# Kernel tuning notes

Measured on AMD Instinct MI355X. Metric: run time of the kernel, lower is better.

Reference implementation:

```python
import jax, jax.numpy as jnp
import numpy as np
from jax.scipy.special import gammaln

T, G, M = 730, 2000, 4
NEARZERO = 1e-5
UH_LEN = 15

PHY_NAMES = ['inf_pc','inf_hbv_beta','inf_vic_bexp','inf_hmets_alpha','sr_soil_depth_1',
 'bf1_gr4j_x3','bf1_pl_bfc','bf1_pl_bfn','bf1_vic_bfmax','bf1_vic_bfn','bf1_top_bfmax',
 'bf1_top_bfn','bf1_top_lam','bf1_thresh_bfmax','bf1_thresh_bfn','bf1_thresh_bfthresh',
 'perc_gawser_maxperc','crise_hbv_crise','bf2_con_bfmax','bf2_gr4j_x3','bf2_lin_bfc',
 'bf2_pl_bfc','bf2_pl_bfn','bf2_vic_bfmax','bf2_vic_bfn',
 'ddf','Tbm','Tbf','cfr','swi','vadose_max_level']
PHY_BOUNDS = np.array([[0.,1.],[0.5,3.],[0.001,3.],[0.3,1.],[0.05,0.5],
 [20.,300.],[0.001,0.5],[1.,5.],[0.1,50.],[1.,5.],[0.1,50.],
 [1.,5.],[5.,10.],[0.1,50.],[1.,5.],[0.,1.],
 [1.,50.],[0.1,50.],[0.1,50.],[20.,300.],[0.0001,0.1],
 [0.0001,0.1],[1.,5.],[0.1,50.],[1.,5.],
 [0.,20.],[-2.,3.],[-5.,2.],[0.,1.],[0.05,0.4],[10.,500.]], dtype=np.float32)
ROUT_BOUNDS = np.array([[0.3,20.],[0.01,5.],[0.5,13.],[0.15,1.5]], dtype=np.float32)


def uh_gamma(a, theta, L):
    # gamma-distribution unit hydrograph, a/theta: [G] -> [G, L]
    aa = jax.nn.relu(a) + 0.1
    th = jax.nn.relu(theta) + 0.5
    t = jnp.arange(0.5, float(L))  # [L]
    logw = (aa[:, None] - 1.0) * jnp.log(t)[None, :] - t[None, :] / th[:, None] \
           - gammaln(aa)[:, None] - aa[:, None] * jnp.log(th[:, None])
    w = jnp.exp(logw)
    return w / jnp.sum(w, axis=1, keepdims=True)


def route(q, uh):
    # causal per-basin convolution: q [T,G], uh [G,L] -> [T,G]
    L = uh.shape[1]
    x = q.T[None]                 # [1, G, T]
    k = uh[:, None, ::-1]         # [G, 1, L]  (reversed -> true convolution)
    out = jax.lax.conv_general_dilated(x, k, window_strides=(1,),
                                       padding=[(L - 1, 0)],
                                       feature_group_count=G,
                                       dimension_numbers=('NCW', 'OIW', 'NCW'))
    return out[0].T


def _model(x_phy, weights_params, hybrid_params):
    P = len(PHY_NAMES)
    lb = jnp.asarray(PHY_BOUNDS[:, 0]); ub = jnp.asarray(PHY_BOUNDS[:, 1])
    phy = jax.nn.sigmoid(hybrid_params[:, :P * M].reshape(G, P, M))
    phy = lb[None, :, None] + phy * (ub - lb)[None, :, None]       # [G,P,M]
    pd = {n: phy[:, i, :] for i, n in enumerate(PHY_NAMES)}
    rb = jnp.asarray(ROUT_BOUNDS)
    rout = jax.nn.sigmoid(hybrid_params[:, P * M:P * M + 4])
    rout = rb[:, 0][None] + rout * (rb[:, 1] - rb[:, 0])[None]      # [G,4]
    a1, b1, a2, b2 = rout[:, 0], rout[:, 1], rout[:, 2], rout[:, 3]
    # 9 blend weights, softmax within the 3 groups of 3
    w = jax.nn.softmax(weights_params.reshape(T, G, 3, 3, M), axis=3)
    vmax = pd['vadose_max_level']                                   # [G,M]

    def step(carry, xs):
        snow, liqw, cum, vad, phr = carry
        prcp, temp, pet, wt = xs           # [G],[G],[G],[G,3,3,M]
        p = prcp[:, None]; tt = temp[:, None]; pe = pet[:, None]    # [G,M]
        rain = p * (tt >= 0.0)
        snowf = p * (tt < 0.0)
        # --- snow module: 3 parallel snowpacks (HMETS/HBV/VIC style) ---
        t3 = tt[..., None]
        snow = snow + snowf[..., None]
        ddf = pd['ddf'][..., None]
        one = jnp.ones_like(cum[..., 0])
        fac = jnp.stack([one, one, jnp.minimum(1.0 + cum[..., 2] / 100.0, 2.0)], axis=-1)
        melt = jnp.minimum(ddf * fac * jax.nn.relu(t3 - pd['Tbm'][..., None]), snow)
        refr = jnp.minimum(pd['cfr'][..., None] * ddf * jax.nn.relu(pd['Tbf'][..., None] - t3), liqw)
        snow = snow - melt + refr
        liqw = liqw + melt - refr
        cap = pd['swi'][..., None] * snow
        release = jax.nn.relu(liqw - cap)
        liqw = jnp.minimum(liqw, cap)
        cum = jnp.where(snow > 10.0 * NEARZERO, cum + melt, 0.0)
        water = rain + jnp.mean(release, axis=-1)                    # [G,M]
        # --- infiltration: blend of HMETS / HBV / VIC (weights group 1) ---
        sm = jnp.clip(vad / vmax, 1e-4, 1.0 - 1e-4)
        i1 = pd['inf_hmets_alpha'] * water * (1.0 - sm)
        i2 = water * (1.0 - sm ** pd['inf_hbv_beta'])
        i3 = water * (1.0 - sm) ** pd['inf_vic_bexp']
        w1 = wt[:, 0]
        infil = w1[:, 0] * i1 + w1[:, 1] * i2 + w1[:, 2] * i3
        runoff = jax.nn.relu(water - infil)
        # --- baseflow 1 from vadose zone (weights group 2) ---
        q1 = vad * (1.0 - (1.0 + (vad / pd['bf1_gr4j_x3']) ** 4) ** (-0.25))
        q2 = pd['bf1_pl_bfc'] * vmax * sm ** pd['bf1_pl_bfn']
        q3 = pd['bf1_vic_bfmax'] * sm ** pd['bf1_vic_bfn']
        w2 = wt[:, 1]
        bf1 = jnp.minimum(w2[:, 0] * q1 + w2[:, 1] * q2 + w2[:, 2] * q3, vad)
        perc = pd['perc_gawser_maxperc'] * sm
        crise = jnp.minimum(pd['crise_hbv_crise'] * (1.0 - sm), phr)
        aet = pe * sm
        vad_new = vad + infil + crise - bf1 - perc - aet
        over = jax.nn.relu(vad_new - vmax)
        vad = jnp.clip(vad_new, NEARZERO, vmax)
        runoff = runoff + over
        # --- baseflow 2 from phreatic zone (weights group 3) ---
        c1 = jnp.minimum(pd['bf2_con_bfmax'], phr)
        c2 = pd['bf2_lin_bfc'] * phr
        c3 = pd['bf2_vic_bfmax'] * (phr / (phr + pd['bf2_gr4j_x3'])) ** pd['bf2_vic_bfn']
        w3 = wt[:, 2]
        bf2 = jnp.minimum(w3[:, 0] * c1 + w3[:, 1] * c2 + w3[:, 2] * c3, phr)
        phr = jnp.maximum(phr + perc - crise - bf2, NEARZERO)
        outs = (jnp.mean(runoff, -1), jnp.mean(bf1 + bf2, -1),
                jnp.mean(aet, -1), jnp.mean(vad, -1), jnp.mean(phr, -1))
        return (snow, liqw, cum, vad, phr), outs

    s0 = jnp.full((G, M, 3), NEARZERO, dtype=x_phy.dtype)
    carry0 = (s0, s0, s0, 0.5 * vmax, jnp.full((G, M), NEARZERO, dtype=x_phy.dtype))
    xs = (x_phy[:, :, 0], x_phy[:, :, 1], x_phy[:, :, 2], w)
    _, (qk, qb, aet_s, vad_s, phr_s) = jax.lax.scan(step, carry0, xs)
    uh1 = uh_gamma(a1, b1, UH_LEN)
    uh2 = uh_gamma(a2, b2, UH_LEN)
    Q = route(qk, uh1) + route(qb, uh2)   # [T,G]
    return Q, aet_s, vad_s, phr_s


def setup_inputs() -> dict:
    key = jax.random.key(0)
    k1, k2, k3, k4, k5 = jax.random.split(key, 5)
    prcp = jax.nn.relu(jax.random.normal(k1, (T, G)) * 5.0)
    temp = jax.random.normal(k2, (T, G)) * 8.0 + 2.0
    pet = jax.random.uniform(k3, (T, G)) * 5.0
    x_phy = jnp.stack([prcp, temp, pet], axis=-1).astype(jnp.float32)
    weights_params = jax.random.normal(k4, (T, G, 9 * M), dtype=jnp.float32)
    hybrid_params = jax.random.normal(k5, (G, len(PHY_NAMES) * M + 4), dtype=jnp.float32)
    return {'x_phy': x_phy, 'weights_params': weights_params, 'hybrid_params': hybrid_params}


def reference(x_phy, weights_params, hybrid_params):
    return _model(x_phy, weights_params, hybrid_params)
```

## Files before the change

### kernel.cpp

```cpp
#include <hip/hip_runtime.h>


#define TS 730
#define GC 2000
#define MM 4
#define TG (TS*GC)

__device__ __forceinline__ float fexp(float x){ return __expf(x); }
__device__ __forceinline__ float flog(float x){ return __logf(x); }
__device__ __forceinline__ float frcp(float x){ return __builtin_amdgcn_rcpf(x); }

__device__ __forceinline__ float qsum(float x){
    x += __shfl_xor(x, 1, 64);
    x += __shfl_xor(x, 2, 64);
    return x;
}

__global__ __launch_bounds__(64, 1) void scan_kernel(
    const float* __restrict__ x_phy,
    const float* __restrict__ wts,
    const float* __restrict__ hyb,
    float* __restrict__ out,
    float* __restrict__ qk,
    float* __restrict__ qb)
{
    const int tid = blockIdx.x*64 + threadIdx.x;
    const int g = tid >> 2, m = tid & 3;

    const float* hp = hyb + g*128 + m;
    #define PARAM(i, lo, hi) ((lo) + ((hi)-(lo)) / (1.0f + __expf(-hp[(i)*4])))
    const float beta    = PARAM(1,  0.5f,   3.0f);
    const float bexp    = PARAM(2,  0.001f, 3.0f);
    const float alpha   = PARAM(3,  0.3f,   1.0f);
    const float x3      = PARAM(5,  20.0f,  300.0f);
    const float plbfc   = PARAM(6,  0.001f, 0.5f);
    const float plbfn   = PARAM(7,  1.0f,   5.0f);
    const float vbmax   = PARAM(8,  0.1f,   50.0f);
    const float vbfn    = PARAM(9,  1.0f,   5.0f);
    const float maxperc = PARAM(16, 1.0f,   50.0f);
    const float crise_p = PARAM(17, 0.1f,   50.0f);
    const float c_bfmax = PARAM(18, 0.1f,   50.0f);
    const float g4x3    = PARAM(19, 20.0f,  300.0f);
    const float linbfc  = PARAM(20, 1e-4f,  0.1f);
    const float b2vmax  = PARAM(23, 0.1f,   50.0f);
    const float b2vn    = PARAM(24, 1.0f,   5.0f);
    const float ddf     = PARAM(25, 0.0f,   20.0f);
    const float Tbm     = PARAM(26, -2.0f,  3.0f);
    const float Tbf     = PARAM(27, -5.0f,  2.0f);
    const float cfr     = PARAM(28, 0.0f,   1.0f);
    const float swi     = PARAM(29, 0.05f,  0.4f);
    const float vmax    = PARAM(30, 10.0f,  500.0f);
    #undef PARAM

    const float inv_vmax = 1.0f / vmax;
    const float inv_x3   = 1.0f / x3;
    const float cfr_ddf  = cfr * ddf;
    const float q2c      = plbfc * vmax;

    float snow0 = 1e-5f, snow1 = 1e-5f, snow2 = 1e-5f;
    float liqw0 = 1e-5f, liqw1 = 1e-5f, liqw2 = 1e-5f;
    float cum0  = 1e-5f, cum1  = 1e-5f, cum2  = 1e-5f;
    float vad = 0.5f * vmax;
    float phr = 1e-5f;

    const float* xp0 = x_phy + g*3;
    const float* wp0 = wts + g*36 + m;
    float p = xp0[0], tt = xp0[1], pe = xp0[2];
    float r0 = wp0[0],  r1 = wp0[4],  r2 = wp0[8];
    float r3 = wp0[12], r4 = wp0[16], r5 = wp0[20];
    float r6 = wp0[24], r7 = wp0[28], r8 = wp0[32];

    for (int t = 0; t < TS; ++t) {
        const int tn = (t+1 < TS) ? (t+1) : t;
        const float* xn = x_phy + tn*(GC*3)  + g*3;
        const float* wn = wts   + tn*(GC*36) + g*36 + m;
        const float np = xn[0], ntt = xn[1], npe = xn[2];
        const float n0 = wn[0],  n1 = wn[4],  n2 = wn[8];
        const float n3 = wn[12], n4 = wn[16], n5 = wn[20];
        const float n6 = wn[24], n7 = wn[28], n8 = wn[32];

        const float e0=fexp(r0), e1=fexp(r1), e2=fexp(r2);
        const float e3=fexp(r3), e4=fexp(r4), e5=fexp(r5);
        const float e6=fexp(r6), e7=fexp(r7), e8=fexp(r8);
        const float is1 = frcp(e0+e1+e2);
        const float is2 = frcp(e3+e4+e5);
        const float is3 = frcp(e6+e7+e8);

        const float rain  = (tt >= 0.0f) ? p : 0.0f;
        const float snowf = (tt <  0.0f) ? p : 0.0f;
        const float meltb = ddf     * fmaxf(tt - Tbm, 0.0f);
        const float refrb = cfr_ddf * fmaxf(Tbf - tt, 0.0f);
        const float fac2  = fminf(1.0f + cum2*0.01f, 2.0f);

        float rel0, rel1, rel2;
        {
            snow0 += snowf;
            const float melt = fminf(meltb, snow0);
            const float refr = fminf(refrb, liqw0);
            snow0 = snow0 - melt + refr;
            liqw0 = liqw0 + melt - refr;
            const float cap = swi*snow0;
            rel0 = fmaxf(liqw0 - cap, 0.0f);
            liqw0 = fminf(liqw0, cap);
            cum0 = (snow0 > 1e-4f) ? cum0 + melt : 0.0f;
        }
        {
            snow1 += snowf;
            const float melt = fminf(meltb, snow1);
            const float refr = fminf(refrb, liqw1);
            snow1 = snow1 - melt + refr;
            liqw1 = liqw1 + melt - refr;
            const float cap = swi*snow1;
            rel1 = fmaxf(liqw1 - cap, 0.0f);
            liqw1 = fminf(liqw1, cap);
            cum1 = (snow1 > 1e-4f) ? cum1 + melt : 0.0f;
        }
        {
            snow2 += snowf;
            const float melt = fminf(meltb*fac2, snow2);
            const float refr = fminf(refrb, liqw2);
            snow2 = snow2 - melt + refr;
            liqw2 = liqw2 + melt - refr;
            const float cap = swi*snow2;
            rel2 = fmaxf(liqw2 - cap, 0.0f);
            liqw2 = fminf(liqw2, cap);
            cum2 = (snow2 > 1e-4f) ? cum2 + melt : 0.0f;
        }

        const float water = rain + (rel0+rel1+rel2)*(1.0f/3.0f);

        const float sm     = fminf(fmaxf(vad*inv_vmax, 1e-4f), 1.0f - 1e-4f);
        const float one_sm = 1.0f - sm;
        const float lsm    = flog(sm);
        const float l1sm   = flog(one_sm);
        const float i1 = alpha * water * one_sm;
        const float i2 = water * (1.0f - fexp(beta*lsm));
        const float i3 = water * fexp(bexp*l1sm);
        const float infil = (e0*i1 + e1*i2 + e2*i3) * is1;
        float runoff = fmaxf(water - infil, 0.0f);

        const float y   = vad * inv_x3;
        const float y2  = y*y;
        const float b14 = 1.0f + y2*y2;
        const float q1  = vad * (1.0f - rsqrtf(sqrtf(b14)));
        const float q2  = q2c   * fexp(plbfn*lsm);
        const float q3  = vbmax * fexp(vbfn*lsm);
        const float bf1 = fminf((e3*q1 + e4*q2 + e5*q3) * is2, vad);

        const float perc  = maxperc * sm;
        const float crise = fminf(crise_p * one_sm, phr);
        const float aet   = pe * sm;
        const float vad_new = vad + infil + crise - bf1 - perc - aet;
        const float over  = fmaxf(vad_new - vmax, 0.0f);
        vad = fminf(fmaxf(vad_new, 1e-5f), vmax);
        runoff += over;

        const float c1 = fminf(c_bfmax, phr);
        const float c2 = linbfc * phr;
        const float fr = phr * frcp(phr + g4x3);
        const float c3 = b2vmax * fexp(b2vn * flog(fr));
        const float bf2 = fminf((e6*c1 + e7*c2 + e8*c3) * is3, phr);
        phr = fmaxf(phr + perc - crise - bf2, 1e-5f);

        const float s_run = qsum(runoff);
        const float s_qb  = qsum(bf1 + bf2);
        const float s_aet = qsum(aet);
        const float s_vad = qsum(vad);
        const float s_phr = qsum(phr);
        if (m == 0) {
            const int o = t*GC + g;
            qk[o]         = s_run*0.25f;
            qb[o]         = s_qb *0.25f;
            out[TG   + o] = s_aet*0.25f;
            out[2*TG + o] = s_vad*0.25f;
            out[3*TG + o] = s_phr*0.25f;
        }

        p = np; tt = ntt; pe = npe;
        r0=n0; r1=n1; r2=n2; r3=n3; r4=n4; r5=n5; r6=n6; r7=n7; r8=n8;
    }
}

__global__ __launch_bounds__(64) void uh_kernel(
    const float* __restrict__ hyb, float* __restrict__ uh1, float* __restrict__ uh2)
{
    const int g = blockIdx.x*64 + threadIdx.x;
    if (g >= GC) return;
    const float* hp = hyb + g*128 + 124;
    const float s0 = 1.0f/(1.0f + __expf(-hp[0]));
    const float s1 = 1.0f/(1.0f + __expf(-hp[1]));
    const float s2 = 1.0f/(1.0f + __expf(-hp[2]));
    const float s3 = 1.0f/(1.0f + __expf(-hp[3]));
    const float a1 = 0.3f  + (20.0f-0.3f) *s0;
    const float b1 = 0.01f + (5.0f-0.01f) *s1;
    const float a2 = 0.5f  + (13.0f-0.5f) *s2;
    const float b2 = 0.15f + (1.5f-0.15f) *s3;

    #pragma unroll
    for (int which = 0; which < 2; ++which) {
        const float a  = which ? a2 : a1;
        const float th = which ? b2 : b1;
        float* dst = which ? uh2 : uh1;
        const float aa = fmaxf(a, 0.0f) + 0.1f;
        const float tv_inv = 1.0f / (fmaxf(th, 0.0f) + 0.5f);
        float lw[15]; float mx = -1e30f;
        #pragma unroll
        for (int l = 0; l < 15; ++l) {
            const float tv = (float)l + 0.5f;
            lw[l] = (aa - 1.0f)*__logf(tv) - tv*tv_inv;
            mx = fmaxf(mx, lw[l]);
        }
        float w[15]; float s = 0.0f;
        #pragma unroll
        for (int l = 0; l < 15; ++l) { w[l] = __expf(lw[l]-mx); s += w[l]; }
        const float inv_s = 1.0f/s;
        #pragma unroll
        for (int l = 0; l < 15; ++l) dst[l*GC + g] = w[l]*inv_s;
    }
}

__global__ __launch_bounds__(256) void route_kernel(
    const float* __restrict__ qk, const float* __restrict__ qb,
    const float* __restrict__ uh1, const float* __restrict__ uh2,
    float* __restrict__ Q)
{
    const int tid = blockIdx.x*256 + threadIdx.x;
    if (tid >= TG) return;
    const int t = tid / GC;
    const int g = tid - t*GC;
    float acc = 0.0f;
    if (t >= 14) {
        #pragma unroll
        for (int l = 0; l < 15; ++l) {
            const int o = tid - l*GC;
            acc += qk[o]*uh1[l*GC+g] + qb[o]*uh2[l*GC+g];
        }
    } else {
        for (int l = 0; l <= t; ++l) {
            const int o = tid - l*GC;
            acc += qk[o]*uh1[l*GC+g] + qb[o]*uh2[l*GC+g];
        }
    }
    Q[tid] = acc;
}

extern "C" void kernel_launch(void* const* d_in, const int* in_sizes, int n_in,
                              void* d_out, int out_size, void* d_ws, size_t ws_size,
                              hipStream_t stream)
{
    const float* x_phy = (const float*)d_in[0];
    const float* wts   = (const float*)d_in[1];
    const float* hyb   = (const float*)d_in[2];
    float* out = (float*)d_out;
    float* ws  = (float*)d_ws;
    float* qk  = ws;
    float* qb  = ws + TG;
    float* uh1 = ws + 2*TG;
    float* uh2 = ws + 2*TG + 15*GC;

    uh_kernel   <<<(GC+63)/64,   64,  0, stream>>>(hyb, uh1, uh2);
    scan_kernel <<<(GC*MM)/64,   64,  0, stream>>>(x_phy, wts, hyb, out, qk, qb);
    route_kernel<<<(TG+255)/256, 256, 0, stream>>>(qk, qb, uh1, uh2, out);
}
```

Baseline: 747.9 us.

## Deepen input prefetch to five steps and use DPP for quad reductions

The time loop is now unrolled by five, with a five-slot register ring buffer. Each step's forcing and weight loads are issued five iterations ahead, so global memory latency is hidden behind more of the serial recurrence. The quad reduction also swaps ds_swizzle/shfl for DPP quad-permute moves, which shortens the cross-lane latency on the critical path. In exchange, register pressure rises by about 60 VGPRs for the buffered slots. TS=730 is divisible by 5, so no remainder step is needed.

```diff
diff --git a/kernel.cpp b/kernel.cpp
--- a/kernel.cpp
+++ b/kernel.cpp
@@ -5,15 +5,17 @@
 #define GC 2000
 #define MM 4
 #define TG (TS*GC)
+#define PD 5
 
 __device__ __forceinline__ float fexp(float x){ return __expf(x); }
 __device__ __forceinline__ float flog(float x){ return __logf(x); }
 __device__ __forceinline__ float frcp(float x){ return __builtin_amdgcn_rcpf(x); }
 
 __device__ __forceinline__ float qsum(float x){
-    x += __shfl_xor(x, 1, 64);
-    x += __shfl_xor(x, 2, 64);
-    return x;
+    float y = __int_as_float(__builtin_amdgcn_mov_dpp(__float_as_int(x), 0xB1, 0xF, 0xF, true));
+    x += y;
+    y = __int_as_float(__builtin_amdgcn_mov_dpp(__float_as_int(x), 0x4E, 0xF, 0xF, true));
+    return x + y;
 }
 
 __global__ __launch_bounds__(64, 1) void scan_kernel(
@@ -63,122 +65,129 @@
     float vad = 0.5f * vmax;
     float phr = 1e-5f;
 
-    const float* xp0 = x_phy + g*3;
-    const float* wp0 = wts + g*36 + m;
-    float p = xp0[0], tt = xp0[1], pe = xp0[2];
-    float r0 = wp0[0],  r1 = wp0[4],  r2 = wp0[8];
-    float r3 = wp0[12], r4 = wp0[16], r5 = wp0[20];
-    float r6 = wp0[24], r7 = wp0[28], r8 = wp0[32];
-
-    for (int t = 0; t < TS; ++t) {
-        const int tn = (t+1 < TS) ? (t+1) : t;
-        const float* xn = x_phy + tn*(GC*3)  + g*3;
-        const float* wn = wts   + tn*(GC*36) + g*36 + m;
-        const float np = xn[0], ntt = xn[1], npe = xn[2];
-        const float n0 = wn[0],  n1 = wn[4],  n2 = wn[8];
-        const float n3 = wn[12], n4 = wn[16], n5 = wn[20];
-        const float n6 = wn[24], n7 = wn[28], n8 = wn[32];
-
-        const float e0=fexp(r0), e1=fexp(r1), e2=fexp(r2);
-        const float e3=fexp(r3), e4=fexp(r4), e5=fexp(r5);
-        const float e6=fexp(r6), e7=fexp(r7), e8=fexp(r8);
-        const float is1 = frcp(e0+e1+e2);
-        const float is2 = frcp(e3+e4+e5);
-        const float is3 = frcp(e6+e7+e8);
-
-        const float rain  = (tt >= 0.0f) ? p : 0.0f;
-        const float snowf = (tt <  0.0f) ? p : 0.0f;
-        const float meltb = ddf     * fmaxf(tt - Tbm, 0.0f);
-        const float refrb = cfr_ddf * fmaxf(Tbf - tt, 0.0f);
-        const float fac2  = fminf(1.0f + cum2*0.01f, 2.0f);
-
-        float rel0, rel1, rel2;
-        {
-            snow0 += snowf;
-            const float melt = fminf(meltb, snow0);
-            const float refr = fminf(refrb, liqw0);
-            snow0 = snow0 - melt + refr;
-            liqw0 = liqw0 + melt - refr;
-            const float cap = swi*snow0;
-            rel0 = fmaxf(liqw0 - cap, 0.0f);
-            liqw0 = fminf(liqw0, cap);
-            cum0 = (snow0 > 1e-4f) ? cum0 + melt : 0.0f;
-        }
-        {
-            snow1 += snowf;
-            const float melt = fminf(meltb, snow1);
-            const float refr = fminf(refrb, liqw1);
-            snow1 = snow1 - melt + refr;
-            liqw1 = liqw1 + melt - refr;
-            const float cap = swi*snow1;
-            rel1 = fmaxf(liqw1 - cap, 0.0f);
-            liqw1 = fminf(liqw1, cap);
-            cum1 = (snow1 > 1e-4f) ? cum1 + melt : 0.0f;
-        }
-        {
-            snow2 += snowf;
-            const float melt = fminf(meltb*fac2, snow2);
-            const float refr = fminf(refrb, liqw2);
-            snow2 = snow2 - melt + refr;
-            liqw2 = liqw2 + melt - refr;
-            const float cap = swi*snow2;
-            rel2 = fmaxf(liqw2 - cap, 0.0f);
-            liqw2 = fminf(liqw2, cap);
-            cum2 = (snow2 > 1e-4f) ? cum2 + melt : 0.0f;
-        }
-
-        const float water = rain + (rel0+rel1+rel2)*(1.0f/3.0f);
-
-        const float sm     = fminf(fmaxf(vad*inv_vmax, 1e-4f), 1.0f - 1e-4f);
-        const float one_sm = 1.0f - sm;
-        const float lsm    = flog(sm);
-        const float l1sm   = flog(one_sm);
-        const float i1 = alpha * water * one_sm;
-        const float i2 = water * (1.0f - fexp(beta*lsm));
-        const float i3 = water * fexp(bexp*l1sm);
-        const float infil = (e0*i1 + e1*i2 + e2*i3) * is1;
-        float runoff = fmaxf(water - infil, 0.0f);
-
-        const float y   = vad * inv_x3;
-        const float y2  = y*y;
-        const float b14 = 1.0f + y2*y2;
-        const float q1  = vad * (1.0f - rsqrtf(sqrtf(b14)));
-        const float q2  = q2c   * fexp(plbfn*lsm);
-        const float q3  = vbmax * fexp(vbfn*lsm);
-        const float bf1 = fminf((e3*q1 + e4*q2 + e5*q3) * is2, vad);
-
-        const float perc  = maxperc * sm;
-        const float crise = fminf(crise_p * one_sm, phr);
-        const float aet   = pe * sm;
-        const float vad_new = vad + infil + crise - bf1 - perc - aet;
-        const float over  = fmaxf(vad_new - vmax, 0.0f);
-        vad = fminf(fmaxf(vad_new, 1e-5f), vmax);
-        runoff += over;
-
-        const float c1 = fminf(c_bfmax, phr);
-        const float c2 = linbfc * phr;
-        const float fr = phr * frcp(phr + g4x3);
-        const float c3 = b2vmax * fexp(b2vn * flog(fr));
-        const float bf2 = fminf((e6*c1 + e7*c2 + e8*c3) * is3, phr);
-        phr = fmaxf(phr + perc - crise - bf2, 1e-5f);
-
-        const float s_run = qsum(runoff);
-        const float s_qb  = qsum(bf1 + bf2);
-        const float s_aet = qsum(aet);
-        const float s_vad = qsum(vad);
-        const float s_phr = qsum(phr);
-        if (m == 0) {
-            const int o = t*GC + g;
-            qk[o]         = s_run*0.25f;
-            qb[o]         = s_qb *0.25f;
-            out[TG   + o] = s_aet*0.25f;
-            out[2*TG + o] = s_vad*0.25f;
-            out[3*TG + o] = s_phr*0.25f;
-        }
-
-        p = np; tt = ntt; pe = npe;
-        r0=n0; r1=n1; r2=n2; r3=n3; r4=n4; r5=n5; r6=n6; r7=n7; r8=n8;
+    float fp[PD], ft[PD], fe[PD], w_[PD][9];
+    #define LOAD_SLOT(k, tn) { \
+        const float* xn = x_phy + (tn)*(GC*3)  + g*3; \
+        const float* wn = wts   + (tn)*(GC*36) + g*36 + m; \
+        fp[k]=xn[0]; ft[k]=xn[1]; fe[k]=xn[2]; \
+        w_[k][0]=wn[0];  w_[k][1]=wn[4];  w_[k][2]=wn[8]; \
+        w_[k][3]=wn[12]; w_[k][4]=wn[16]; w_[k][5]=wn[20]; \
+        w_[k][6]=wn[24]; w_[k][7]=wn[28]; w_[k][8]=wn[32]; }
+
+    #pragma unroll
+    for (int k = 0; k < PD; ++k) LOAD_SLOT(k, k);
+
+    for (int tb = 0; tb < TS; tb += PD) {
+        #pragma unroll
+        for (int k = 0; k < PD; ++k) {
+            const int t = tb + k;
+
+            const float p  = fp[k], tt = ft[k], pe = fe[k];
+            const float r0 = w_[k][0], r1 = w_[k][1], r2 = w_[k][2];
+            const float r3 = w_[k][3], r4 = w_[k][4], r5 = w_[k][5];
+            const float r6 = w_[k][6], r7 = w_[k][7], r8 = w_[k][8];
+            int tn = t + PD; if (tn >= TS) tn = TS - 1;
+            LOAD_SLOT(k, tn);
+
+            const float e0=fexp(r0), e1=fexp(r1), e2=fexp(r2);
+            const float e3=fexp(r3), e4=fexp(r4), e5=fexp(r5);
+            const float e6=fexp(r6), e7=fexp(r7), e8=fexp(r8);
+            const float is1 = frcp(e0+e1+e2);
+            const float is2 = frcp(e3+e4+e5);
+            const float is3 = frcp(e6+e7+e8);
+
+            const float rain  = (tt >= 0.0f) ? p : 0.0f;
+            const float snowf = (tt <  0.0f) ? p : 0.0f;
+            const float meltb = ddf     * fmaxf(tt - Tbm, 0.0f);
+            const float refrb = cfr_ddf * fmaxf(Tbf - tt, 0.0f);
+            const float fac2  = fminf(1.0f + cum2*0.01f, 2.0f);
+
+            float rel0, rel1, rel2;
+            {
+                snow0 += snowf;
+                const float melt = fminf(meltb, snow0);
+                const float refr = fminf(refrb, liqw0);
+                snow0 = snow0 - melt + refr;
+                liqw0 = liqw0 + melt - refr;
+                const float cap = swi*snow0;
+                rel0 = fmaxf(liqw0 - cap, 0.0f);
+                liqw0 = fminf(liqw0, cap);
+                cum0 = (snow0 > 1e-4f) ? cum0 + melt : 0.0f;
+            }
+            {
+                snow1 += snowf;
+                const float melt = fminf(meltb, snow1);
+                const float refr = fminf(refrb, liqw1);
+                snow1 = snow1 - melt + refr;
+                liqw1 = liqw1 + melt - refr;
+                const float cap = swi*snow1;
+                rel1 = fmaxf(liqw1 - cap, 0.0f);
+                liqw1 = fminf(liqw1, cap);
+                cum1 = (snow1 > 1e-4f) ? cum1 + melt : 0.0f;
+            }
+            {
+                snow2 += snowf;
+                const float melt = fminf(meltb*fac2, snow2);
+                const float refr = fminf(refrb, liqw2);
+                snow2 = snow2 - melt + refr;
+                liqw2 = liqw2 + melt - refr;
+                const float cap = swi*snow2;
+                rel2 = fmaxf(liqw2 - cap, 0.0f);
+                liqw2 = fminf(liqw2, cap);
+                cum2 = (snow2 > 1e-4f) ? cum2 + melt : 0.0f;
+            }
+
+            const float water = rain + (rel0+rel1+rel2)*(1.0f/3.0f);
+
+            const float sm     = fminf(fmaxf(vad*inv_vmax, 1e-4f), 1.0f - 1e-4f);
+            const float one_sm = 1.0f - sm;
+            const float lsm    = flog(sm);
+            const float l1sm   = flog(one_sm);
+            const float i1 = alpha * water * one_sm;
+            const float i2 = water * (1.0f - fexp(beta*lsm));
+            const float i3 = water * fexp(bexp*l1sm);
+            const float infil = (e0*i1 + e1*i2 + e2*i3) * is1;
+            float runoff = fmaxf(water - infil, 0.0f);
+
+            const float y   = vad * inv_x3;
+            const float y2  = y*y;
+            const float b14 = 1.0f + y2*y2;
+            const float q1  = vad * (1.0f - rsqrtf(sqrtf(b14)));
+            const float q2  = q2c   * fexp(plbfn*lsm);
+            const float q3  = vbmax * fexp(vbfn*lsm);
+            const float bf1 = fminf((e3*q1 + e4*q2 + e5*q3) * is2, vad);
+
+            const float perc  = maxperc * sm;
+            const float crise = fminf(crise_p * one_sm, phr);
+            const float aet   = pe * sm;
+            const float vad_new = vad + infil + crise - bf1 - perc - aet;
+            const float over  = fmaxf(vad_new - vmax, 0.0f);
+            vad = fminf(fmaxf(vad_new, 1e-5f), vmax);
+            runoff += over;
+
+            const float c1 = fminf(c_bfmax, phr);
+            const float c2 = linbfc * phr;
+            const float fr = phr * frcp(phr + g4x3);
+            const float c3 = b2vmax * fexp(b2vn * flog(fr));
+            const float bf2 = fminf((e6*c1 + e7*c2 + e8*c3) * is3, phr);
+            phr = fmaxf(phr + perc - crise - bf2, 1e-5f);
+
+            const float s_run = qsum(runoff);
+            const float s_qb  = qsum(bf1 + bf2);
+            const float s_aet = qsum(aet);
+            const float s_vad = qsum(vad);
+            const float s_phr = qsum(phr);
+            if (m == 0) {
+                const int o = t*GC + g;
+                qk[o]         = s_run*0.25f;
+                qb[o]         = s_qb *0.25f;
+                out[TG   + o] = s_aet*0.25f;
+                out[2*TG + o] = s_vad*0.25f;
+                out[3*TG + o] = s_phr*0.25f;
+            }
+        }
     }
+    #undef LOAD_SLOT
 }
 
 __global__ __launch_bounds__(64) void uh_kernel(
```

Result: faster. 665.2 us (-11.1%).
